# Performance work log

Measured on AMD Instinct MI355X. Metric: run time of the kernel, lower is better.

The kernel has to match this reference:

```python
import jax, jax.numpy as jnp
import numpy as np

N = 256
MAX_LENGTH = 1024
BATCH = 32768


def _transition(n):
    # HiPPO-LegS transition matrices (float64 numpy, matches torch module)
    q = np.arange(n, dtype=np.float64)
    col, row = np.meshgrid(q, q)
    r = 2 * q + 1
    M = -(np.where(row >= col, r, 0) - np.diag(q))
    T = np.sqrt(np.diag(2 * q + 1))
    A = T @ M @ np.linalg.inv(T)
    B = np.diag(T)  # squeezed (N,)
    return A, B


def _build_stacked(n, max_length):
    # Bilinear (Tustin) discretization at every timescale t=1..max_length.
    A, B = _transition(n)
    ts = np.arange(1, max_length + 1, dtype=np.float64)  # (L,)
    At = A[None] / ts[:, None, None]                     # (L,N,N)
    Bt = B[None] / ts[:, None]                           # (L,N)
    I = np.eye(n)
    lhs = I[None] - At / 2                               # (L,N,N), lower triangular
    A_stacked = np.linalg.solve(lhs, I[None] + At / 2)   # (L,N,N)
    B_stacked = np.linalg.solve(lhs, Bt[..., None])[..., 0]  # (L,N)
    return A_stacked.astype(np.float32), B_stacked.astype(np.float32)


def setup_inputs() -> dict:
    key = jax.random.key(0)
    k1, k2 = jax.random.split(key)
    A_np, B_np = _build_stacked(N, MAX_LENGTH)
    return {
        "c": jax.random.normal(k1, (BATCH, N), dtype=jnp.float32),
        "f": jax.random.normal(k2, (BATCH, 1), dtype=jnp.float32),
        "A_stacked": jnp.asarray(A_np),  # (L, N, N) buffer
        "B_stacked": jnp.asarray(B_np),  # (L, N) buffer
        "t": 512,
    }


def reference(c, f, A_stacked, B_stacked, t):
    # F.linear(c, A) == c @ A.T ; then scaled add of new value f
    A = A_stacked[t]            # (N, N)
    b = B_stacked[t]            # (N,)
    return c @ A.T + b * f      # (BATCH, N)
```

## Files before the change

kernel.cpp:

```cpp
#include <hip/hip_runtime.h>
#include <cstdint>
#include <cstddef>

typedef _Float16 half8 __attribute__((ext_vector_type(8)));
typedef float f32x4 __attribute__((ext_vector_type(4)));

static constexpr int kN   = 256;
static constexpr int kKS  = 8;
static constexpr int kNTb = 8;
static constexpr int kBM  = 128;
static constexpr size_t kABytes = (size_t)kN * kN * 2;
static constexpr size_t kLDS    = kABytes / 2;

__global__ __launch_bounds__(256) void hippo_prep(
    const float* __restrict__ A_stacked, const int* __restrict__ tptr,
    _Float16* __restrict__ a16)
{
    const int t = tptr[0];
    const float* __restrict__ A = A_stacked + (size_t)t * kN * kN;
    const int tid = blockIdx.x * 256 + threadIdx.x;
    const int nt = tid >> 9;
    const int ks = (tid >> 6) & 7;
    const int l  = tid & 63;
    const int row = nt * 16 + (l & 15);
    const int k0  = ks * 32 + ((l >> 4) << 3);
    const float* __restrict__ src = A + row * kN + k0;
    f32x4 v0 = *(const f32x4*)(src);
    f32x4 v1 = *(const f32x4*)(src + 4);
    half8 h;
    h[0] = (_Float16)v0[0]; h[1] = (_Float16)v0[1];
    h[2] = (_Float16)v0[2]; h[3] = (_Float16)v0[3];
    h[4] = (_Float16)v1[0]; h[5] = (_Float16)v1[1];
    h[6] = (_Float16)v1[2]; h[7] = (_Float16)v1[3];
    ((half8*)a16)[tid] = h;
}

__global__ __launch_bounds__(512, 4) void hippo_gemm(
    const float* __restrict__ c, const float* __restrict__ f,
    const float* __restrict__ Bst, const int* __restrict__ tptr,
    const _Float16* __restrict__ a16, float* __restrict__ out)
{
    extern __shared__ char lds_raw[];

    const int tid  = threadIdx.x;
    const int l    = tid & 63;
    const int wid  = tid >> 6;
    const int lo16 = l & 15;
    const int hi4  = l >> 4;

    const int bid = blockIdx.x;
    const int mb  = bid & 255;
    const int nh  = bid >> 8;
    const int m0  = mb * kBM + wid * 16;
    const int n0  = nh * 128;

    const float* __restrict__ cptr = c + (size_t)(m0 + lo16) * kN + (hi4 << 3);
    f32x4 cv0[kKS], cv1[kKS];
    #pragma unroll
    for (int ks = 0; ks < kKS; ++ks) {
        cv0[ks] = *(const f32x4*)(cptr + ks * 32);
        cv1[ks] = *(const f32x4*)(cptr + ks * 32 + 4);
    }

    const int t = tptr[0];
    const float* __restrict__ brow = Bst + (size_t)t * kN + n0;
    float bvs[kNTb];
    #pragma unroll
    for (int nt = 0; nt < kNTb; ++nt) bvs[nt] = brow[nt * 16 + lo16];
    float fv[4];
    #pragma unroll
    for (int r = 0; r < 4; ++r) fv[r] = f[m0 + (hi4 << 2) + r];

    {
        const char* __restrict__ gsrc = (const char*)a16 + (size_t)nh * kLDS;
        #pragma unroll
        for (int i = 0; i < 8; ++i) {
            const int chunk = i * 8 + wid;
            const size_t off = (size_t)chunk * 1024 + (size_t)l * 16;
            __builtin_amdgcn_global_load_lds(
                (const __attribute__((address_space(1))) void*)(gsrc + off),
                (__attribute__((address_space(3))) void*)(lds_raw + off),
                16, 0, 0);
        }
    }

    half8 af[kKS];
    #pragma unroll
    for (int ks = 0; ks < kKS; ++ks) {
        af[ks][0] = (_Float16)cv0[ks][0]; af[ks][1] = (_Float16)cv0[ks][1];
        af[ks][2] = (_Float16)cv0[ks][2]; af[ks][3] = (_Float16)cv0[ks][3];
        af[ks][4] = (_Float16)cv1[ks][0]; af[ks][5] = (_Float16)cv1[ks][1];
        af[ks][6] = (_Float16)cv1[ks][2]; af[ks][7] = (_Float16)cv1[ks][3];
    }

    __syncthreads();

    f32x4 acc[kNTb];
    #pragma unroll
    for (int i = 0; i < kNTb; ++i) acc[i] = (f32x4){0.f, 0.f, 0.f, 0.f};

    const half8* __restrict__ Bs = (const half8*)lds_raw;
    #pragma unroll
    for (int ks = 0; ks < kKS; ++ks) {
        #pragma unroll
        for (int nt = 0; nt < kNTb; ++nt) {
            half8 bf = Bs[(nt * kKS + ks) * 64 + l];
            acc[nt] = __builtin_amdgcn_mfma_f32_16x16x32_f16(af[ks], bf, acc[nt], 0, 0, 0);
        }
    }

    float* __restrict__ obase = out + (size_t)(m0 + (hi4 << 2)) * kN + n0 + lo16;
    #pragma unroll
    for (int nt = 0; nt < kNTb; ++nt) {
        #pragma unroll
        for (int r = 0; r < 4; ++r)
            obase[(size_t)r * kN + nt * 16] = acc[nt][r] + bvs[nt] * fv[r];
    }
}

extern "C" void kernel_launch(void* const* d_in, const int* in_sizes, int n_in,
                              void* d_out, int out_size, void* d_ws, size_t ws_size,
                              hipStream_t stream) {
    const float* c   = (const float*)d_in[0];
    const float* f   = (const float*)d_in[1];
    const float* A   = (const float*)d_in[2];
    const float* B   = (const float*)d_in[3];
    const int*   t   = (const int*)d_in[4];
    float* out = (float*)d_out;
    _Float16* a16 = (_Float16*)d_ws;

    const int batch = in_sizes[0] / kN;

    hipFuncSetAttribute((const void*)hippo_gemm,
                        hipFuncAttributeMaxDynamicSharedMemorySize,
                        (int)kLDS);

    hipLaunchKernelGGL(hippo_prep, dim3(32), dim3(256), 0, stream, A, t, a16);
    hipLaunchKernelGGL(hippo_gemm, dim3((batch / kBM) * 2), dim3(512), kLDS, stream,
                       c, f, B, t, a16, out);
}
```

Before: 26.58 us.

## Compute full N per block with K split into two LDS-staged halves

Result: faster. 22.87 us (-14.0%).

```diff
diff --git a/kernel.cpp b/kernel.cpp
--- a/kernel.cpp
+++ b/kernel.cpp
@@ -5,12 +5,10 @@
 typedef _Float16 half8 __attribute__((ext_vector_type(8)));
 typedef float f32x4 __attribute__((ext_vector_type(4)));
 
-static constexpr int kN   = 256;
-static constexpr int kKS  = 8;
-static constexpr int kNTb = 8;
-static constexpr int kBM  = 128;
-static constexpr size_t kABytes = (size_t)kN * kN * 2;
-static constexpr size_t kLDS    = kABytes / 2;
+static constexpr int kN  = 256;
+static constexpr int kBM = 64;
+static constexpr size_t kHalfB  = 64 * 1024;
+static constexpr size_t kLDS    = kHalfB;
 
 __global__ __launch_bounds__(256) void hippo_prep(
     const float* __restrict__ A_stacked, const int* __restrict__ tptr,
@@ -19,12 +17,13 @@
     const int t = tptr[0];
     const float* __restrict__ A = A_stacked + (size_t)t * kN * kN;
     const int tid = blockIdx.x * 256 + threadIdx.x;
-    const int nt = tid >> 9;
-    const int ks = (tid >> 6) & 7;
-    const int l  = tid & 63;
+    const int ksh = tid >> 12;
+    const int nt  = (tid >> 8) & 15;
+    const int ks2 = (tid >> 6) & 3;
+    const int l   = tid & 63;
     const int row = nt * 16 + (l & 15);
-    const int k0  = ks * 32 + ((l >> 4) << 3);
-    const float* __restrict__ src = A + row * kN + k0;
+    const int k0  = (ksh * 4 + ks2) * 32 + ((l >> 4) << 3);
+    const float* __restrict__ src = A + (size_t)row * kN + k0;
     f32x4 v0 = *(const f32x4*)(src);
     f32x4 v1 = *(const f32x4*)(src + 4);
     half8 h;
@@ -35,7 +34,7 @@
     ((half8*)a16)[tid] = h;
 }
 
-__global__ __launch_bounds__(512, 4) void hippo_gemm(
+__global__ __launch_bounds__(256, 2) void hippo_gemm(
     const float* __restrict__ c, const float* __restrict__ f,
     const float* __restrict__ Bst, const int* __restrict__ tptr,
     const _Float16* __restrict__ a16, float* __restrict__ out)
@@ -47,71 +46,101 @@
     const int wid  = tid >> 6;
     const int lo16 = l & 15;
     const int hi4  = l >> 4;
+    const int bid  = blockIdx.x;
+    const int m0   = bid * kBM + wid * 16;
+    const int hA   = bid & 1;
+    const int hB   = hA ^ 1;
 
-    const int bid = blockIdx.x;
-    const int mb  = bid & 255;
-    const int nh  = bid >> 8;
-    const int m0  = mb * kBM + wid * 16;
-    const int n0  = nh * 128;
+    const char* __restrict__ gsrcA = (const char*)a16 + (size_t)hA * kHalfB;
+    #pragma unroll
+    for (int i = 0; i < 16; ++i) {
+        const size_t off = (size_t)(i * 4 + wid) * 1024 + (size_t)l * 16;
+        __builtin_amdgcn_global_load_lds(
+            (const __attribute__((address_space(1))) void*)(gsrcA + off),
+            (__attribute__((address_space(3))) void*)(lds_raw + off),
+            16, 0, 0);
+    }
 
     const float* __restrict__ cptr = c + (size_t)(m0 + lo16) * kN + (hi4 << 3);
-    f32x4 cv0[kKS], cv1[kKS];
+    f32x4 cv0[4], cv1[4];
     #pragma unroll
-    for (int ks = 0; ks < kKS; ++ks) {
-        cv0[ks] = *(const f32x4*)(cptr + ks * 32);
-        cv1[ks] = *(const f32x4*)(cptr + ks * 32 + 4);
+    for (int ks = 0; ks < 4; ++ks) {
+        cv0[ks] = *(const f32x4*)(cptr + hA * 128 + ks * 32);
+        cv1[ks] = *(const f32x4*)(cptr + hA * 128 + ks * 32 + 4);
     }
 
     const int t = tptr[0];
-    const float* __restrict__ brow = Bst + (size_t)t * kN + n0;
-    float bvs[kNTb];
+    const float* __restrict__ brow = Bst + (size_t)t * kN;
+    float bvs[16];
     #pragma unroll
-    for (int nt = 0; nt < kNTb; ++nt) bvs[nt] = brow[nt * 16 + lo16];
+    for (int nt = 0; nt < 16; ++nt) bvs[nt] = brow[nt * 16 + lo16];
     float fv[4];
     #pragma unroll
     for (int r = 0; r < 4; ++r) fv[r] = f[m0 + (hi4 << 2) + r];
 
-    {
-        const char* __restrict__ gsrc = (const char*)a16 + (size_t)nh * kLDS;
-        #pragma unroll
-        for (int i = 0; i < 8; ++i) {
-            const int chunk = i * 8 + wid;
-            const size_t off = (size_t)chunk * 1024 + (size_t)l * 16;
-            __builtin_amdgcn_global_load_lds(
-                (const __attribute__((address_space(1))) void*)(gsrc + off),
-                (__attribute__((address_space(3))) void*)(lds_raw + off),
-                16, 0, 0);
-        }
-    }
+    __syncthreads();
 
-    half8 af[kKS];
+    half8 af[4];
     #pragma unroll
-    for (int ks = 0; ks < kKS; ++ks) {
+    for (int ks = 0; ks < 4; ++ks) {
         af[ks][0] = (_Float16)cv0[ks][0]; af[ks][1] = (_Float16)cv0[ks][1];
         af[ks][2] = (_Float16)cv0[ks][2]; af[ks][3] = (_Float16)cv0[ks][3];
         af[ks][4] = (_Float16)cv1[ks][0]; af[ks][5] = (_Float16)cv1[ks][1];
         af[ks][6] = (_Float16)cv1[ks][2]; af[ks][7] = (_Float16)cv1[ks][3];
     }
-
-    __syncthreads();
-
-    f32x4 acc[kNTb];
+    const half8* __restrict__ Bs = (const half8*)lds_raw;
+    f32x4 acc[16];
     #pragma unroll
-    for (int i = 0; i < kNTb; ++i) acc[i] = (f32x4){0.f, 0.f, 0.f, 0.f};
-
-    const half8* __restrict__ Bs = (const half8*)lds_raw;
+    for (int i = 0; i < 16; ++i) acc[i] = (f32x4){0.f, 0.f, 0.f, 0.f};
     #pragma unroll
-    for (int ks = 0; ks < kKS; ++ks) {
+    for (int ks = 0; ks < 4; ++ks) {
         #pragma unroll
-        for (int nt = 0; nt < kNTb; ++nt) {
-            half8 bf = Bs[(nt * kKS + ks) * 64 + l];
+        for (int nt = 0; nt < 16; ++nt) {
+            half8 bf = Bs[(nt * 4 + ks) * 64 + l];
             acc[nt] = __builtin_amdgcn_mfma_f32_16x16x32_f16(af[ks], bf, acc[nt], 0, 0, 0);
         }
     }
 
-    float* __restrict__ obase = out + (size_t)(m0 + (hi4 << 2)) * kN + n0 + lo16;
+    __syncthreads();
+
+    const char* __restrict__ gsrcB = (const char*)a16 + (size_t)hB * kHalfB;
     #pragma unroll
-    for (int nt = 0; nt < kNTb; ++nt) {
+    for (int i = 0; i < 16; ++i) {
+        const size_t off = (size_t)(i * 4 + wid) * 1024 + (size_t)l * 16;
+        __builtin_amdgcn_global_load_lds(
+            (const __attribute__((address_space(1))) void*)(gsrcB + off),
+            (__attribute__((address_space(3))) void*)(lds_raw + off),
+            16, 0, 0);
+    }
+    f32x4 dv0[4], dv1[4];
+    #pragma unroll
+    for (int ks = 0; ks < 4; ++ks) {
+        dv0[ks] = *(const f32x4*)(cptr + hB * 128 + ks * 32);
+        dv1[ks] = *(const f32x4*)(cptr + hB * 128 + ks * 32 + 4);
+    }
+
+    __syncthreads();
+
+    half8 ag[4];
+    #pragma unroll
+    for (int ks = 0; ks < 4; ++ks) {
+        ag[ks][0] = (_Float16)dv0[ks][0]; ag[ks][1] = (_Float16)dv0[ks][1];
+        ag[ks][2] = (_Float16)dv0[ks][2]; ag[ks][3] = (_Float16)dv0[ks][3];
+        ag[ks][4] = (_Float16)dv1[ks][0]; ag[ks][5] = (_Float16)dv1[ks][1];
+        ag[ks][6] = (_Float16)dv1[ks][2]; ag[ks][7] = (_Float16)dv1[ks][3];
+    }
+    #pragma unroll
+    for (int ks = 0; ks < 4; ++ks) {
+        #pragma unroll
+        for (int nt = 0; nt < 16; ++nt) {
+            half8 bf = Bs[(nt * 4 + ks) * 64 + l];
+            acc[nt] = __builtin_amdgcn_mfma_f32_16x16x32_f16(ag[ks], bf, acc[nt], 0, 0, 0);
+        }
+    }
+
+    float* __restrict__ obase = out + (size_t)(m0 + (hi4 << 2)) * kN + lo16;
+    #pragma unroll
+    for (int nt = 0; nt < 16; ++nt) {
         #pragma unroll
         for (int r = 0; r < 4; ++r)
             obase[(size_t)r * kN + nt * 16] = acc[nt][r] + bvs[nt] * fv[r];
@@ -136,6 +165,6 @@
                         (int)kLDS);
 
     hipLaunchKernelGGL(hippo_prep, dim3(32), dim3(256), 0, stream, A, t, a16);
-    hipLaunchKernelGGL(hippo_gemm, dim3((batch / kBM) * 2), dim3(512), kLDS, stream,
+    hipLaunchKernelGGL(hippo_gemm, dim3(batch / kBM), dim3(256), kLDS, stream,
                        c, f, B, t, a16, out);
 }
```

## Load full fp16 A into LDS per block and process two M-tiles per wave

Applied to the files above, without the earlier changes.

New measurement: 25.82 us. 2.9% less time.

```diff
diff --git a/kernel.cpp b/kernel.cpp
--- a/kernel.cpp
+++ b/kernel.cpp
@@ -5,12 +5,9 @@
 typedef _Float16 half8 __attribute__((ext_vector_type(8)));
 typedef float f32x4 __attribute__((ext_vector_type(4)));
 
-static constexpr int kN   = 256;
-static constexpr int kKS  = 8;
-static constexpr int kNTb = 8;
-static constexpr int kBM  = 128;
+static constexpr int kN  = 256;
+static constexpr int kKS = 8;
 static constexpr size_t kABytes = (size_t)kN * kN * 2;
-static constexpr size_t kLDS    = kABytes / 2;
 
 __global__ __launch_bounds__(256) void hippo_prep(
     const float* __restrict__ A_stacked, const int* __restrict__ tptr,
@@ -35,7 +32,7 @@
     ((half8*)a16)[tid] = h;
 }
 
-__global__ __launch_bounds__(512, 4) void hippo_gemm(
+__global__ __launch_bounds__(512, 2) void hippo_gemm(
     const float* __restrict__ c, const float* __restrict__ f,
     const float* __restrict__ Bst, const int* __restrict__ tptr,
     const _Float16* __restrict__ a16, float* __restrict__ out)
@@ -45,43 +42,51 @@
     const int tid  = threadIdx.x;
     const int l    = tid & 63;
     const int wid  = tid >> 6;
+    const int wm   = wid & 3;
+    const int wn   = wid >> 2;
     const int lo16 = l & 15;
     const int hi4  = l >> 4;
+    const int m0   = blockIdx.x * 128 + wm * 16;
+    const int m1   = m0 + 64;
+    const int ntb  = wn * 8;
 
-    const int bid = blockIdx.x;
-    const int mb  = bid & 255;
-    const int nh  = bid >> 8;
-    const int m0  = mb * kBM + wid * 16;
-    const int n0  = nh * 128;
-
-    const float* __restrict__ cptr = c + (size_t)(m0 + lo16) * kN + (hi4 << 3);
+    const float* __restrict__ cp0 = c + (size_t)(m0 + lo16) * kN + (hi4 << 3);
     f32x4 cv0[kKS], cv1[kKS];
     #pragma unroll
     for (int ks = 0; ks < kKS; ++ks) {
-        cv0[ks] = *(const f32x4*)(cptr + ks * 32);
-        cv1[ks] = *(const f32x4*)(cptr + ks * 32 + 4);
+        cv0[ks] = *(const f32x4*)(cp0 + ks * 32);
+        cv1[ks] = *(const f32x4*)(cp0 + ks * 32 + 4);
+    }
+
+    #pragma unroll
+    for (int i = 0; i < 16; ++i) {
+        const size_t off = (size_t)(i * 8 + wid) * 1024 + (size_t)l * 16;
+        __builtin_amdgcn_global_load_lds(
+            (const __attribute__((address_space(1))) void*)((const char*)a16 + off),
+            (__attribute__((address_space(3))) void*)(lds_raw + off),
+            16, 0, 0);
     }
 
     const int t = tptr[0];
-    const float* __restrict__ brow = Bst + (size_t)t * kN + n0;
-    float bvs[kNTb];
+    const float* __restrict__ brow = Bst + (size_t)t * kN + wn * 128;
+    float bvs[8];
     #pragma unroll
-    for (int nt = 0; nt < kNTb; ++nt) bvs[nt] = brow[nt * 16 + lo16];
-    float fv[4];
+    for (int nt = 0; nt < 8; ++nt) bvs[nt] = brow[nt * 16 + lo16];
+    float fv0[4], fv1[4];
     #pragma unroll
-    for (int r = 0; r < 4; ++r) fv[r] = f[m0 + (hi4 << 2) + r];
+    for (int r = 0; r < 4; ++r) {
+        fv0[r] = f[m0 + (hi4 << 2) + r];
+        fv1[r] = f[m1 + (hi4 << 2) + r];
+    }
 
-    {
-        const char* __restrict__ gsrc = (const char*)a16 + (size_t)nh * kLDS;
-        #pragma unroll
-        for (int i = 0; i < 8; ++i) {
-            const int chunk = i * 8 + wid;
-            const size_t off = (size_t)chunk * 1024 + (size_t)l * 16;
-            __builtin_amdgcn_global_load_lds(
-                (const __attribute__((address_space(1))) void*)(gsrc + off),
-                (__attribute__((address_space(3))) void*)(lds_raw + off),
-                16, 0, 0);
-        }
+    __syncthreads();
+
+    const float* __restrict__ cp1 = c + (size_t)(m1 + lo16) * kN + (hi4 << 3);
+    f32x4 dv0[kKS], dv1[kKS];
+    #pragma unroll
+    for (int ks = 0; ks < kKS; ++ks) {
+        dv0[ks] = *(const f32x4*)(cp1 + ks * 32);
+        dv1[ks] = *(const f32x4*)(cp1 + ks * 32 + 4);
     }
 
     half8 af[kKS];
@@ -92,29 +97,51 @@
         af[ks][4] = (_Float16)cv1[ks][0]; af[ks][5] = (_Float16)cv1[ks][1];
         af[ks][6] = (_Float16)cv1[ks][2]; af[ks][7] = (_Float16)cv1[ks][3];
     }
-
-    __syncthreads();
-
-    f32x4 acc[kNTb];
+    const half8* __restrict__ Bs = (const half8*)lds_raw;
+    f32x4 acc[8];
     #pragma unroll
-    for (int i = 0; i < kNTb; ++i) acc[i] = (f32x4){0.f, 0.f, 0.f, 0.f};
-
-    const half8* __restrict__ Bs = (const half8*)lds_raw;
+    for (int i = 0; i < 8; ++i) acc[i] = (f32x4){0.f, 0.f, 0.f, 0.f};
     #pragma unroll
     for (int ks = 0; ks < kKS; ++ks) {
         #pragma unroll
-        for (int nt = 0; nt < kNTb; ++nt) {
-            half8 bf = Bs[(nt * kKS + ks) * 64 + l];
+        for (int nt = 0; nt < 8; ++nt) {
+            half8 bf = Bs[((ntb + nt) * kKS + ks) * 64 + l];
             acc[nt] = __builtin_amdgcn_mfma_f32_16x16x32_f16(af[ks], bf, acc[nt], 0, 0, 0);
         }
     }
-
-    float* __restrict__ obase = out + (size_t)(m0 + (hi4 << 2)) * kN + n0 + lo16;
+    float* __restrict__ ob0 = out + (size_t)(m0 + (hi4 << 2)) * kN + wn * 128 + lo16;
     #pragma unroll
-    for (int nt = 0; nt < kNTb; ++nt) {
+    for (int nt = 0; nt < 8; ++nt) {
         #pragma unroll
         for (int r = 0; r < 4; ++r)
-            obase[(size_t)r * kN + nt * 16] = acc[nt][r] + bvs[nt] * fv[r];
+            ob0[(size_t)r * kN + nt * 16] = acc[nt][r] + bvs[nt] * fv0[r];
+    }
+
+    half8 ag[kKS];
+    #pragma unroll
+    for (int ks = 0; ks < kKS; ++ks) {
+        ag[ks][0] = (_Float16)dv0[ks][0]; ag[ks][1] = (_Float16)dv0[ks][1];
+        ag[ks][2] = (_Float16)dv0[ks][2]; ag[ks][3] = (_Float16)dv0[ks][3];
+        ag[ks][4] = (_Float16)dv1[ks][0]; ag[ks][5] = (_Float16)dv1[ks][1];
+        ag[ks][6] = (_Float16)dv1[ks][2]; ag[ks][7] = (_Float16)dv1[ks][3];
+    }
+    f32x4 acc2[8];
+    #pragma unroll
+    for (int i = 0; i < 8; ++i) acc2[i] = (f32x4){0.f, 0.f, 0.f, 0.f};
+    #pragma unroll
+    for (int ks = 0; ks < kKS; ++ks) {
+        #pragma unroll
+        for (int nt = 0; nt < 8; ++nt) {
+            half8 bf = Bs[((ntb + nt) * kKS + ks) * 64 + l];
+            acc2[nt] = __builtin_amdgcn_mfma_f32_16x16x32_f16(ag[ks], bf, acc2[nt], 0, 0, 0);
+        }
+    }
+    float* __restrict__ ob1 = out + (size_t)(m1 + (hi4 << 2)) * kN + wn * 128 + lo16;
+    #pragma unroll
+    for (int nt = 0; nt < 8; ++nt) {
+        #pragma unroll
+        for (int r = 0; r < 4; ++r)
+            ob1[(size_t)r * kN + nt * 16] = acc2[nt][r] + bvs[nt] * fv1[r];
     }
 }
 
@@ -133,9 +160,9 @@
 
     hipFuncSetAttribute((const void*)hippo_gemm,
                         hipFuncAttributeMaxDynamicSharedMemorySize,
-                        (int)kLDS);
+                        (int)kABytes);
 
     hipLaunchKernelGGL(hippo_prep, dim3(32), dim3(256), 0, stream, A, t, a16);
-    hipLaunchKernelGGL(hippo_gemm, dim3((batch / kBM) * 2), dim3(512), kLDS, stream,
+    hipLaunchKernelGGL(hippo_gemm, dim3(batch / 128), dim3(512), kABytes, stream,
                        c, f, B, t, a16, out);
 }
```
